# Kernel optimization log

Hardware: AMD Instinct MI355X
Metric: run time of the kernel (lower is better)

## Reference

```python
import math
import jax, jax.numpy as jnp
import numpy as np

B, H, Nt, Nl, E = 4, 16, 512, 512, 64
P = H * E  # 1024, pre-projection embedding dim


def setup_inputs() -> dict:
    key = jax.random.key(0)
    ks = jax.random.split(key, 8)
    return {
        "projected_u": jax.random.normal(ks[0], (B, H, Nt, P), jnp.float32),
        "projected_b": jax.random.normal(ks[1], (B, H, Nt, 1), jnp.float32),
        "mu": jax.random.normal(ks[2], (B, Nl, P), jnp.float32),
        "logvar": jax.random.normal(ks[3], (B, Nl, P), jnp.float32) * 0.5,
        "pi": jax.random.uniform(ks[4], (B, Nl, 1), jnp.float32, 1e-3, 1.0),
        "w_v": jax.random.normal(ks[5], (H, E, P), jnp.float32) * 0.02,
        "b_v": jax.random.normal(ks[6], (H, E, Nl), jnp.float32) * 0.02,
        "attn_mask": jnp.zeros((B * H, 1, Nl), dtype=bool),  # True = masked
    }


def reference(projected_u, projected_b, mu, logvar, pi, w_v, b_v, attn_mask):
    Bq, Hq, Ntq, Pq = projected_u.shape
    Nlq = mu.shape[1]
    Eq = w_v.shape[1]
    prior_var_u = math.sqrt(Eq)

    var = jnp.exp(logvar)                         # [B,Nl,P]
    biased_var = var + prior_var_u                # [B,Nl,P]

    # float additive mask [B*H,1,Nl]: -inf where attn_mask True or pi<=0
    pi_rep = jnp.repeat(pi, Hq, axis=0)           # [B*H,Nl,1]
    am = jnp.where(attn_mask, -jnp.inf, 0.0)
    am = am + jnp.where(pi_rep.transpose(0, 2, 1) <= 0, -jnp.inf, 0.0)
    masked = jnp.isneginf(am).transpose(0, 2, 1)  # [B*H,Nl,1]

    # scores [B,H,Nt,Nl]
    attn = jnp.einsum('bhmp,bnp->bhmn', projected_u, mu / biased_var) + projected_b

    pi_c = jnp.maximum(pi_rep, jnp.finfo(pi_rep.dtype).tiny)
    t1 = jnp.where(masked, 0.0, jnp.log(pi_c))                                  # [B*H,Nl,1]
    t2 = 0.5 * jnp.sum((mu / jnp.sqrt(biased_var)) ** 2, axis=-1, keepdims=True)  # [B,Nl,1]
    t2 = jnp.repeat(t2, Hq, axis=0)                                             # [B*H,Nl,1]
    t3 = jnp.where(masked, 0.0, jnp.log(jnp.repeat(biased_var, Hq, axis=0)))    # [B*H,Nl,P]
    t3 = jnp.sum(0.5 * t3, axis=-1, keepdims=True)                              # [B*H,Nl,1]

    attn = attn + (t1 - t2 - t3).reshape(Bq, Hq, Nlq, 1).transpose(0, 1, 3, 2)  # [B,H,1,Nl]
    attn = attn + am.reshape(Bq, Hq, 1, Nlq)
    attn = jax.nn.softmax(attn, axis=-1)                                        # [B,H,Nt,Nl]

    # denoised values: interpolation between query projection and means
    out = (jnp.einsum('bhmn,bnp->bhmp', attn, var / biased_var) * projected_u
           + jnp.einsum('bhmn,bnp->bhmp', attn, (prior_var_u / biased_var) * mu))  # [B,H,Nt,P]
    out = (jnp.einsum('bhmp,hep->bhme', out, w_v)
           + jnp.einsum('bhmn,hen->bhme', attn, b_v))                              # [B,H,Nt,E]
    return (out.reshape(Bq * Hq, Ntq, Eq), attn.reshape(Bq * Hq, Ntq, Nlq))
```

## Files before the change

### kernel.cpp

```cpp
#include <hip/hip_runtime.h>
#include <cstdint>
#include <cstddef>
#include <cmath>

#define B_  4
#define H_  16
#define NT  512
#define NL  512
#define E_  64
#define P_  1024
#define HE  1024
#define BH  64

typedef __attribute__((ext_vector_type(8))) short short8;
typedef __attribute__((ext_vector_type(8))) unsigned short ushort8;
typedef __attribute__((ext_vector_type(4))) float f32x4;
typedef unsigned short u16;

#define MFMA(a, b, c) __builtin_amdgcn_mfma_f32_16x16x32_bf16(a, b, c, 0, 0, 0)

static __device__ inline u16 f2bf_rne(float f) {
  unsigned u = __float_as_uint(f);
  unsigned r = u + 0x7FFFu + ((u >> 16) & 1u);
  return (u16)(r >> 16);
}

static __device__ inline void gl_lds16(const void* g, void* l) {
  __builtin_amdgcn_global_load_lds(
      (const __attribute__((address_space(1))) void*)g,
      (__attribute__((address_space(3))) void*)l, 16, 0, 0);
}

__global__ __launch_bounds__(256) void k_precompute(
    const float* __restrict__ mu, const float* __restrict__ logvar,
    const float* __restrict__ pi, u16* __restrict__ mobv_hi,
    u16* __restrict__ mobv_lo, u16* __restrict__ ibv,
    float* __restrict__ bias) {
  const int bn = blockIdx.x;
  const int t = threadIdx.x;
  const size_t base = (size_t)bn * P_;
  float t2 = 0.f, t3 = 0.f;
#pragma unroll
  for (int i = 0; i < P_ / 256; ++i) {
    const int p = t + i * 256;
    const float lv  = logvar[base + p];
    const float v   = expf(lv);
    const float bv  = v + 8.0f;
    const float inv = 1.0f / bv;
    const float m   = mu[base + p];
    const float x   = m * inv;
    const unsigned bits = __float_as_uint(x);
    mobv_hi[base + p] = (u16)(bits >> 16);
    const float r = x - __uint_as_float(bits & 0xFFFF0000u);
    mobv_lo[base + p] = (u16)(__float_as_uint(r) >> 16);
    ibv[base + p] = f2bf_rne(inv);
    t2 += m * x;
    t3 += logf(bv);
  }
  __shared__ float r2[256];
  __shared__ float r3[256];
  r2[t] = t2; r3[t] = t3;
  __syncthreads();
  for (int s = 128; s > 0; s >>= 1) {
    if (t < s) { r2[t] += r2[t + s]; r3[t] += r3[t + s]; }
    __syncthreads();
  }
  if (t == 0) {
    const float pv = pi[bn];
    float bb;
    if (pv <= 0.f) bb = -INFINITY;
    else bb = logf(fmaxf(pv, 1.17549435e-38f)) - 0.5f * r2[0] - 0.5f * r3[0];
    bias[bn] = bb;
  }
}

__global__ __launch_bounds__(256) void k_tr(const u16* __restrict__ ibv,
                                            u16* __restrict__ ibvT) {
  const int b  = blockIdx.z;
  const int p0 = blockIdx.x * 64;
  const int n0 = blockIdx.y * 64;
  const int t  = threadIdx.x;
  __shared__ u16 T[64][65];
  {
    const int ln = t >> 2, lp = (t & 3) * 16;
    const u16* src = ibv + ((size_t)b * NL + n0 + ln) * P_ + p0 + lp;
    const ushort8 v0 = *(const ushort8*)(src);
    const ushort8 v1 = *(const ushort8*)(src + 8);
#pragma unroll
    for (int j = 0; j < 8; ++j) { T[ln][lp + j] = v0[j]; T[ln][lp + 8 + j] = v1[j]; }
  }
  __syncthreads();
  {
    const int lp = t >> 2, ln = (t & 3) * 16;
    u16* dst = ibvT + ((size_t)b * P_ + p0 + lp) * NL + n0 + ln;
    ushort8 o0, o1;
#pragma unroll
    for (int j = 0; j < 8; ++j) { o0[j] = T[ln + j][lp]; o1[j] = T[ln + 8 + j][lp]; }
    *(ushort8*)(dst)     = o0;
    *(ushort8*)(dst + 8) = o1;
  }
}

__global__ __launch_bounds__(256) void k_wvcast(const float* __restrict__ wv,
                                                u16* __restrict__ wvb) {
  const int i = (blockIdx.x * 256 + threadIdx.x) * 4;
  const float4 f = *(const float4*)&wv[i];
  wvb[i + 0] = f2bf_rne(f.x);
  wvb[i + 1] = f2bf_rne(f.y);
  wvb[i + 2] = f2bf_rne(f.z);
  wvb[i + 3] = f2bf_rne(f.w);
}

__global__ __launch_bounds__(256) void k_w2p(
    const u16* __restrict__ mobv_hi, const u16* __restrict__ mobv_lo,
    const u16* __restrict__ wvb, const float* __restrict__ bv_,
    u16* __restrict__ W2pT) {
  const int b    = blockIdx.z;
  const int row0 = blockIdx.x * 64;
  const int col0 = blockIdx.y * 128;
  const int t = threadIdx.x;
  const int wave = t >> 6, lane = t & 63;
  const int l16 = lane & 15, sel = lane >> 4;
  const int mrow = (wave >> 1) * 32, ncol = (wave & 1) * 64;

  __shared__ u16 Ah[64 * 32];
  __shared__ u16 Al[64 * 32];
  __shared__ u16 Bs[128 * 32];

  const u16* Abh = mobv_hi + ((size_t)b * NL + row0) * P_;
  const u16* Abl = mobv_lo + ((size_t)b * NL + row0) * P_;
  const u16* Bb  = wvb + (size_t)col0 * P_;

  f32x4 acc[2][4];
#pragma unroll
  for (int i = 0; i < 2; ++i)
#pragma unroll
    for (int j = 0; j < 4; ++j) acc[i][j] = (f32x4){0.f, 0.f, 0.f, 0.f};

  for (int k0 = 0; k0 < P_; k0 += 32) {
    {
      const int c = t;
      const int row = c >> 2, k8 = (c & 3) ^ ((row >> 1) & 3);
      gl_lds16(Abh + (size_t)row * P_ + k0 + k8 * 8, &Ah[wave * 64 * 8]);
      gl_lds16(Abl + (size_t)row * P_ + k0 + k8 * 8, &Al[wave * 64 * 8]);
    }
#pragma unroll
    for (int i = 0; i < 2; ++i) {
      const int c = t + i * 256;
      const int row = c >> 2, k8 = (c & 3) ^ ((row >> 1) & 3);
      gl_lds16(Bb + (size_t)row * P_ + k0 + k8 * 8,
               &Bs[(i * 256 + wave * 64) * 8]);
    }
    __syncthreads();
    short8 ah[2], al[2], bf[4];
#pragma unroll
    for (int mt = 0; mt < 2; ++mt) {
      const int r = mrow + mt * 16 + l16;
      const int ch = sel ^ ((r >> 1) & 3);
      ah[mt] = *(const short8*)&Ah[r * 32 + ch * 8];
      al[mt] = *(const short8*)&Al[r * 32 + ch * 8];
    }
#pragma unroll
    for (int nt = 0; nt < 4; ++nt) {
      const int r = ncol + nt * 16 + l16;
      const int ch = sel ^ ((r >> 1) & 3);
      bf[nt] = *(const short8*)&Bs[r * 32 + ch * 8];
    }
#pragma unroll
    for (int mt = 0; mt < 2; ++mt)
#pragma unroll
      for (int nt = 0; nt < 4; ++nt) {
        acc[mt][nt] = MFMA(ah[mt], bf[nt], acc[mt][nt]);
        acc[mt][nt] = MFMA(al[mt], bf[nt], acc[mt][nt]);
      }
    __syncthreads();
  }
#pragma unroll
  for (int mt = 0; mt < 2; ++mt) {
    const int nbase = row0 + mrow + mt * 16 + sel * 4;
#pragma unroll
    for (int nt = 0; nt < 4; ++nt) {
      const int he = col0 + ncol + nt * 16 + l16;
      const float4 bvv = *(const float4*)&bv_[(size_t)he * NL + nbase];
      ushort4 o;
      o.x = f2bf_rne(8.0f * acc[mt][nt][0] + bvv.x);
      o.y = f2bf_rne(8.0f * acc[mt][nt][1] + bvv.y);
      o.z = f2bf_rne(8.0f * acc[mt][nt][2] + bvv.z);
      o.w = f2bf_rne(8.0f * acc[mt][nt][3] + bvv.w);
      *(ushort4*)&W2pT[((size_t)b * HE + he) * NL + nbase] = o;
    }
  }
}

__global__ __launch_bounds__(256) void k_scores(
    const float* __restrict__ U, const u16* __restrict__ mobv_hi,
    const u16* __restrict__ mobv_lo, const float* __restrict__ pb,
    const float* __restrict__ bias, const uint8_t* __restrict__ mask,
    float* __restrict__ attn) {
  const int b    = blockIdx.z;
  const int row0 = blockIdx.x * 128;
  const int col0 = blockIdx.y * 128;
  const int t = threadIdx.x;
  const int wave = t >> 6, lane = t & 63;
  const int l16 = lane & 15, sel = lane >> 4;
  const int mrow = wave * 32;

  __shared__ float Af[2][128 * 32];
  __shared__ u16   Bh[2][128 * 32];
  __shared__ u16   Bl[2][128 * 32];

  const float* Ab  = U + ((size_t)b * 8192 + row0) * P_;
  const u16*   Bbh = mobv_hi + ((size_t)b * NL + col0) * P_;
  const u16*   Bbl = mobv_lo + ((size_t)b * NL + col0) * P_;

  f32x4 acc[2][8];
#pragma unroll
  for (int i = 0; i < 2; ++i)
#pragma unroll
    for (int j = 0; j < 8; ++j) acc[i][j] = (f32x4){0.f, 0.f, 0.f, 0.f};

  auto stage = [&](int buf, int k0) {
#pragma unroll
    for (int i = 0; i < 4; ++i) {
      const int c = t + i * 256;
      const int row = c >> 3, k4 = (c & 7) ^ (row & 7);
      gl_lds16(Ab + (size_t)row * P_ + k0 + k4 * 4,
               &Af[buf][(i * 256 + wave * 64) * 4]);
    }
#pragma unroll
    for (int i = 0; i < 2; ++i) {
      const int c = t + i * 256;
      const int row = c >> 2, k8 = (c & 3) ^ ((row >> 1) & 3);
      gl_lds16(Bbh + (size_t)row * P_ + k0 + k8 * 8,
               &Bh[buf][(i * 256 + wave * 64) * 8]);
      gl_lds16(Bbl + (size_t)row * P_ + k0 + k8 * 8,
               &Bl[buf][(i * 256 + wave * 64) * 8]);
    }
  };

  stage(0, 0);
  __syncthreads();
  int cur = 0;
  for (int k0 = 0; k0 < P_; k0 += 32) {
    if (k0 + 32 < P_) stage(cur ^ 1, k0 + 32);

    short8 ah[2], al[2], bh[8], bl[8];
#pragma unroll
    for (int mt = 0; mt < 2; ++mt) {
      const int r = mrow + mt * 16 + l16;
      const int c0 = (sel * 2) ^ (r & 7);
      const int c1 = (sel * 2 + 1) ^ (r & 7);
      const float4 f0 = *(const float4*)&Af[cur][r * 32 + c0 * 4];
      const float4 f1 = *(const float4*)&Af[cur][r * 32 + c1 * 4];
      const float fv[8] = {f0.x, f0.y, f0.z, f0.w, f1.x, f1.y, f1.z, f1.w};
#pragma unroll
      for (int j = 0; j < 8; ++j) {
        const unsigned bits = __float_as_uint(fv[j]);
        ah[mt][j] = (short)(bits >> 16);
        const float rr = fv[j] - __uint_as_float(bits & 0xFFFF0000u);
        al[mt][j] = (short)(__float_as_uint(rr) >> 16);
      }
    }
#pragma unroll
    for (int nt = 0; nt < 8; ++nt) {
      const int r = nt * 16 + l16;
      const int ch = sel ^ ((r >> 1) & 3);
      bh[nt] = *(const short8*)&Bh[cur][r * 32 + ch * 8];
      bl[nt] = *(const short8*)&Bl[cur][r * 32 + ch * 8];
    }
#pragma unroll
    for (int mt = 0; mt < 2; ++mt)
#pragma unroll
      for (int nt = 0; nt < 8; ++nt) {
        acc[mt][nt] = MFMA(ah[mt], bh[nt], acc[mt][nt]);
        acc[mt][nt] = MFMA(ah[mt], bl[nt], acc[mt][nt]);
        acc[mt][nt] = MFMA(al[mt], bh[nt], acc[mt][nt]);
      }
    __syncthreads();
    cur ^= 1;
  }

  const int bh_ = b * H_ + (row0 >> 9);
  float pbv[2][4];
#pragma unroll
  for (int mt = 0; mt < 2; ++mt)
#pragma unroll
    for (int r = 0; r < 4; ++r)
      pbv[mt][r] = pb[(size_t)b * 8192 + row0 + mrow + mt * 16 + sel * 4 + r];
#pragma unroll
  for (int nt = 0; nt < 8; ++nt) {
    const int n = col0 + nt * 16 + l16;
    const float bcol = bias[b * NL + n];
    const bool mk = mask[(size_t)bh_ * NL + n] != 0;
#pragma unroll
    for (int mt = 0; mt < 2; ++mt) {
#pragma unroll
      for (int r = 0; r < 4; ++r) {
        const int row = row0 + mrow + mt * 16 + sel * 4 + r;
        float s = acc[mt][nt][r] + pbv[mt][r] + bcol;
        if (mk) s = -INFINITY;
        attn[((size_t)b * 8192 + row) * NL + n] = s;
      }
    }
  }
}

__global__ __launch_bounds__(256) void k_softmax(float* __restrict__ attn,
                                                 u16* __restrict__ attn_bf) {
  const int t = threadIdx.x;
  const int wave = t >> 6, lane = t & 63;
  const size_t r = (size_t)blockIdx.x * 4 + wave;
  float* row = attn + r * NL;
  const float4 v0 = ((const float4*)row)[lane * 2];
  const float4 v1 = ((const float4*)row)[lane * 2 + 1];
  float m = fmaxf(fmaxf(fmaxf(v0.x, v0.y), fmaxf(v0.z, v0.w)),
                  fmaxf(fmaxf(v1.x, v1.y), fmaxf(v1.z, v1.w)));
#pragma unroll
  for (int off = 32; off > 0; off >>= 1) m = fmaxf(m, __shfl_xor(m, off, 64));
  float e[8];
  e[0] = expf(v0.x - m); e[1] = expf(v0.y - m);
  e[2] = expf(v0.z - m); e[3] = expf(v0.w - m);
  e[4] = expf(v1.x - m); e[5] = expf(v1.y - m);
  e[6] = expf(v1.z - m); e[7] = expf(v1.w - m);
  float s = ((e[0] + e[1]) + (e[2] + e[3])) + ((e[4] + e[5]) + (e[6] + e[7]));
#pragma unroll
  for (int off = 32; off > 0; off >>= 1) s += __shfl_xor(s, off, 64);
  const float inv = 1.0f / s;
  float4 o0, o1;
  o0.x = e[0] * inv; o0.y = e[1] * inv; o0.z = e[2] * inv; o0.w = e[3] * inv;
  o1.x = e[4] * inv; o1.y = e[5] * inv; o1.z = e[6] * inv; o1.w = e[7] * inv;
  ((float4*)row)[lane * 2] = o0;
  ((float4*)row)[lane * 2 + 1] = o1;
  ushort4 b0, b1;
  b0.x = f2bf_rne(o0.x); b0.y = f2bf_rne(o0.y);
  b0.z = f2bf_rne(o0.z); b0.w = f2bf_rne(o0.w);
  b1.x = f2bf_rne(o1.x); b1.y = f2bf_rne(o1.y);
  b1.z = f2bf_rne(o1.z); b1.w = f2bf_rne(o1.w);
  ((ushort4*)(attn_bf + r * NL))[lane * 2] = b0;
  ((ushort4*)(attn_bf + r * NL))[lane * 2 + 1] = b1;
}

__global__ __launch_bounds__(256) void k_mid(
    const u16* __restrict__ attn_bf, const u16* __restrict__ ibvT,
    const float* __restrict__ U, u16* __restrict__ opS) {
  const int b    = blockIdx.z;
  const int row0 = blockIdx.x * 128;
  const int col0 = blockIdx.y * 128;
  const int t = threadIdx.x;
  const int wave = t >> 6, lane = t & 63;
  const int l16 = lane & 15, sel = lane >> 4;
  const int mrow = (wave >> 1) * 64, ncol = (wave & 1) * 64;

  __shared__ u16 As[128 * 32];
  __shared__ u16 Bs[128 * 32];

  const u16* Ab = attn_bf + ((size_t)b * 8192 + row0) * NL;
  const u16* Bb = ibvT + ((size_t)b * P_ + col0) * NL;

  f32x4 acc[4][4];
#pragma unroll
  for (int i = 0; i < 4; ++i)
#pragma unroll
    for (int j = 0; j < 4; ++j) acc[i][j] = (f32x4){0.f, 0.f, 0.f, 0.f};

  for (int k0 = 0; k0 < NL; k0 += 32) {
#pragma unroll
    for (int i = 0; i < 2; ++i) {
      const int c = t + i * 256;
      const int row = c >> 2, k8 = (c & 3) ^ ((row >> 1) & 3);
      gl_lds16(Ab + (size_t)row * NL + k0 + k8 * 8,
               &As[(i * 256 + wave * 64) * 8]);
      gl_lds16(Bb + (size_t)row * NL + k0 + k8 * 8,
               &Bs[(i * 256 + wave * 64) * 8]);
    }
    __syncthreads();
    short8 af[4], bf[4];
#pragma unroll
    for (int mt = 0; mt < 4; ++mt) {
      const int r = mrow + mt * 16 + l16;
      const int ch = sel ^ ((r >> 1) & 3);
      af[mt] = *(const short8*)&As[r * 32 + ch * 8];
    }
#pragma unroll
    for (int nt = 0; nt < 4; ++nt) {
      const int r = ncol + nt * 16 + l16;
      const int ch = sel ^ ((r >> 1) & 3);
      bf[nt] = *(const short8*)&Bs[r * 32 + ch * 8];
    }
#pragma unroll
    for (int mt = 0; mt < 4; ++mt)
#pragma unroll
      for (int nt = 0; nt < 4; ++nt)
        acc[mt][nt] = MFMA(af[mt], bf[nt], acc[mt][nt]);
    __syncthreads();
  }

#pragma unroll
  for (int mt = 0; mt < 4; ++mt) {
#pragma unroll
    for (int r = 0; r < 4; ++r) {
      const int m = row0 + mrow + mt * 16 + sel * 4 + r;
      const float* Urow = U + ((size_t)b * 8192 + m) * P_;
      u16* orow = opS + ((size_t)b * 8192 + m) * P_;
#pragma unroll
      for (int nt = 0; nt < 4; ++nt) {
        const int p = col0 + ncol + nt * 16 + l16;
        const float u = Urow[p];
        orow[p] = f2bf_rne((1.0f - 8.0f * acc[mt][nt][r]) * u);
      }
    }
  }
}

__global__ __launch_bounds__(256) void k_out2(
    const u16* __restrict__ opS, const u16* __restrict__ attn_bf,
    const u16* __restrict__ wvb, const u16* __restrict__ W2pT,
    float* __restrict__ out) {
  const int bh = blockIdx.y;
  const int b = bh >> 4, h = bh & 15;
  const int row0g = bh * NT + blockIdx.x * 64;
  const int t = threadIdx.x;
  const int wave = t >> 6, lane = t & 63;
  const int l16 = lane & 15, sel = lane >> 4;
  const int mrow = (wave >> 1) * 32, ncol = (wave & 1) * 32;

  __shared__ u16 As[64 * 64];
  __shared__ u16 Bs[64 * 64];

  f32x4 acc[2][2];
#pragma unroll
  for (int i = 0; i < 2; ++i)
#pragma unroll
    for (int j = 0; j < 2; ++j) acc[i][j] = (f32x4){0.f, 0.f, 0.f, 0.f};

  const u16* Ab1 = opS + (size_t)row0g * P_;
  const u16* Bb1 = wvb + (size_t)(h * 64) * P_;
  for (int k0 = 0; k0 < P_; k0 += 64) {
#pragma unroll
    for (int i = 0; i < 2; ++i) {
      const int c = t + i * 256;
      const int row = c >> 3, k8 = (c & 7) ^ (row & 7);
      gl_lds16(Ab1 + (size_t)row * P_ + k0 + k8 * 8,
               &As[(i * 256 + wave * 64) * 8]);
      gl_lds16(Bb1 + (size_t)row * P_ + k0 + k8 * 8,
               &Bs[(i * 256 + wave * 64) * 8]);
    }
    __syncthreads();
    short8 af[2][2], bf[2][2];
#pragma unroll
    for (int mt = 0; mt < 2; ++mt) {
      const int r = mrow + mt * 16 + l16;
#pragma unroll
      for (int kk = 0; kk < 2; ++kk) {
        const int ch = (kk * 4 + sel) ^ (r & 7);
        af[mt][kk] = *(const short8*)&As[r * 64 + ch * 8];
      }
    }
#pragma unroll
    for (int nt = 0; nt < 2; ++nt) {
      const int r = ncol + nt * 16 + l16;
#pragma unroll
      for (int kk = 0; kk < 2; ++kk) {
        const int ch = (kk * 4 + sel) ^ (r & 7);
        bf[nt][kk] = *(const short8*)&Bs[r * 64 + ch * 8];
      }
    }
#pragma unroll
    for (int mt = 0; mt < 2; ++mt)
#pragma unroll
      for (int nt = 0; nt < 2; ++nt) {
        acc[mt][nt] = MFMA(af[mt][0], bf[nt][0], acc[mt][nt]);
        acc[mt][nt] = MFMA(af[mt][1], bf[nt][1], acc[mt][nt]);
      }
    __syncthreads();
  }

  const u16* Ab2 = attn_bf + (size_t)row0g * NL;
  const u16* Bb2 = W2pT + ((size_t)b * HE + h * 64) * NL;
  for (int k0 = 0; k0 < NL; k0 += 64) {
#pragma unroll
    for (int i = 0; i < 2; ++i) {
      const int c = t + i * 256;
      const int row = c >> 3, k8 = (c & 7) ^ (row & 7);
      gl_lds16(Ab2 + (size_t)row * NL + k0 + k8 * 8,
               &As[(i * 256 + wave * 64) * 8]);
      gl_lds16(Bb2 + (size_t)row * NL + k0 + k8 * 8,
               &Bs[(i * 256 + wave * 64) * 8]);
    }
    __syncthreads();
    short8 af[2][2], bf[2][2];
#pragma unroll
    for (int mt = 0; mt < 2; ++mt) {
      const int r = mrow + mt * 16 + l16;
#pragma unroll
      for (int kk = 0; kk < 2; ++kk) {
        const int ch = (kk * 4 + sel) ^ (r & 7);
        af[mt][kk] = *(const short8*)&As[r * 64 + ch * 8];
      }
    }
#pragma unroll
    for (int nt = 0; nt < 2; ++nt) {
      const int r = ncol + nt * 16 + l16;
#pragma unroll
      for (int kk = 0; kk < 2; ++kk) {
        const int ch = (kk * 4 + sel) ^ (r & 7);
        bf[nt][kk] = *(const short8*)&Bs[r * 64 + ch * 8];
      }
    }
#pragma unroll
    for (int mt = 0; mt < 2; ++mt)
#pragma unroll
      for (int nt = 0; nt < 2; ++nt) {
        acc[mt][nt] = MFMA(af[mt][0], bf[nt][0], acc[mt][nt]);
        acc[mt][nt] = MFMA(af[mt][1], bf[nt][1], acc[mt][nt]);
      }
    __syncthreads();
  }

#pragma unroll
  for (int mt = 0; mt < 2; ++mt)
#pragma unroll
    for (int nt = 0; nt < 2; ++nt)
#pragma unroll
      for (int r = 0; r < 4; ++r) {
        const int row = row0g + mrow + mt * 16 + sel * 4 + r;
        const int e = ncol + nt * 16 + l16;
        out[(size_t)row * E_ + e] = acc[mt][nt][r];
      }
}

extern "C" void kernel_launch(void* const* d_in, const int* in_sizes, int n_in,
                              void* d_out, int out_size, void* d_ws, size_t ws_size,
                              hipStream_t stream) {
  const float*   u    = (const float*)d_in[0];
  const float*   pb   = (const float*)d_in[1];
  const float*   mu   = (const float*)d_in[2];
  const float*   logv = (const float*)d_in[3];
  const float*   pi   = (const float*)d_in[4];
  const float*   wv   = (const float*)d_in[5];
  const float*   bv   = (const float*)d_in[6];
  const uint8_t* mask = (const uint8_t*)d_in[7];

  float* out  = (float*)d_out;
  float* attn = out + (size_t)BH * NT * E_;

  u16*   mobv_hi = (u16*)d_ws;
  u16*   mobv_lo = mobv_hi + (size_t)B_ * NL * P_;
  u16*   ibvT    = mobv_lo + (size_t)B_ * NL * P_;
  u16*   W2pT    = ibvT + (size_t)B_ * P_ * NL;
  u16*   wvb     = W2pT + (size_t)B_ * HE * NL;
  float* bias    = (float*)(wvb + (size_t)HE * P_);
  u16*   attn_bf = (u16*)(bias + (size_t)B_ * NL);
  u16*   opS     = attn_bf + (size_t)BH * NT * NL;
  u16*   ibv     = opS;

  k_precompute<<<B_ * NL, 256, 0, stream>>>(mu, logv, pi, mobv_hi, mobv_lo,
                                            ibv, bias);
  k_tr<<<dim3(P_ / 64, NL / 64, B_), 256, 0, stream>>>(ibv, ibvT);
  k_wvcast<<<(HE * P_) / 1024, 256, 0, stream>>>(wv, wvb);
  k_w2p<<<dim3(NL / 64, HE / 128, B_), 256, 0, stream>>>(mobv_hi, mobv_lo, wvb,
                                                         bv, W2pT);
  k_scores<<<dim3(8192 / 128, NL / 128, B_), 256, 0, stream>>>(
      u, mobv_hi, mobv_lo, pb, bias, mask, attn);
  k_softmax<<<(B_ * H_ * NT) / 4, 256, 0, stream>>>(attn, attn_bf);
  k_mid<<<dim3(8192 / 128, P_ / 128, B_), 256, 0, stream>>>(attn_bf, ibvT, u,
                                                            opS);
  k_out2<<<dim3(NT / 64, BH), 256, 0, stream>>>(opS, attn_bf, wvb, W2pT, out);
}
```

Baseline: 464.9 us.

## Fuse mid and output GEMMs into one kernel, keeping intermediate in LDS

Merges k_mid (attn·ibvT times U) and k_out2 (projection by w_v plus attn·W2pT) into a single kernel. Each block now produces the 64×1024 intermediate in 128-column chunks, writes each chunk to LDS as bf16 and multiplies it straight into the E=64 output accumulator. This removes the global write and reread of the large opS buffer. The trade-off is a smaller 64-row M tile per block, so attn_bf is re-read once for each of the 8 P-chunks, and LDS use grows, which may lower occupancy. Separately, k_precompute is vectorised to float4 loads and ushort4 stores.

```diff
diff --git a/kernel.cpp b/kernel.cpp
--- a/kernel.cpp
+++ b/kernel.cpp
@@ -39,24 +39,37 @@
   const int bn = blockIdx.x;
   const int t = threadIdx.x;
   const size_t base = (size_t)bn * P_;
+  const int p = t * 4;
+  const float4 lv4 = *(const float4*)&logvar[base + p];
+  const float4 m4  = *(const float4*)&mu[base + p];
   float t2 = 0.f, t3 = 0.f;
-#pragma unroll
-  for (int i = 0; i < P_ / 256; ++i) {
-    const int p = t + i * 256;
-    const float lv  = logvar[base + p];
-    const float v   = expf(lv);
-    const float bv  = v + 8.0f;
-    const float inv = 1.0f / bv;
-    const float m   = mu[base + p];
-    const float x   = m * inv;
-    const unsigned bits = __float_as_uint(x);
-    mobv_hi[base + p] = (u16)(bits >> 16);
-    const float r = x - __uint_as_float(bits & 0xFFFF0000u);
-    mobv_lo[base + p] = (u16)(__float_as_uint(r) >> 16);
-    ibv[base + p] = f2bf_rne(inv);
-    t2 += m * x;
-    t3 += logf(bv);
-  }
+  ushort4 ohi, olo, oib;
+  {
+    const float lvv[4] = {lv4.x, lv4.y, lv4.z, lv4.w};
+    const float mvv[4] = {m4.x, m4.y, m4.z, m4.w};
+    u16 hi[4], lo[4], ib[4];
+#pragma unroll
+    for (int j = 0; j < 4; ++j) {
+      const float v   = expf(lvv[j]);
+      const float bv  = v + 8.0f;
+      const float inv = 1.0f / bv;
+      const float m   = mvv[j];
+      const float x   = m * inv;
+      const unsigned bits = __float_as_uint(x);
+      hi[j] = (u16)(bits >> 16);
+      const float r = x - __uint_as_float(bits & 0xFFFF0000u);
+      lo[j] = (u16)(__float_as_uint(r) >> 16);
+      ib[j] = f2bf_rne(inv);
+      t2 += m * x;
+      t3 += logf(bv);
+    }
+    ohi = make_ushort4(hi[0], hi[1], hi[2], hi[3]);
+    olo = make_ushort4(lo[0], lo[1], lo[2], lo[3]);
+    oib = make_ushort4(ib[0], ib[1], ib[2], ib[3]);
+  }
+  *(ushort4*)&mobv_hi[base + p] = ohi;
+  *(ushort4*)&mobv_lo[base + p] = olo;
+  *(ushort4*)&ibv[base + p]     = oib;
   __shared__ float r2[256];
   __shared__ float r3[256];
   r2[t] = t2; r3[t] = t3;
@@ -340,193 +353,121 @@
   ((ushort4*)(attn_bf + r * NL))[lane * 2 + 1] = b1;
 }
 
-__global__ __launch_bounds__(256) void k_mid(
+__global__ __launch_bounds__(256) void k_fused(
     const u16* __restrict__ attn_bf, const u16* __restrict__ ibvT,
-    const float* __restrict__ U, u16* __restrict__ opS) {
-  const int b    = blockIdx.z;
-  const int row0 = blockIdx.x * 128;
-  const int col0 = blockIdx.y * 128;
+    const float* __restrict__ U, const u16* __restrict__ wvb,
+    const u16* __restrict__ W2pT, float* __restrict__ out) {
+  const int bh = blockIdx.y;
+  const int b = bh >> 4, h = bh & 15;
+  const int m0g = bh * NT + blockIdx.x * 64;
   const int t = threadIdx.x;
   const int wave = t >> 6, lane = t & 63;
   const int l16 = lane & 15, sel = lane >> 4;
-  const int mrow = (wave >> 1) * 64, ncol = (wave & 1) * 64;
-
-  __shared__ u16 As[128 * 32];
+  const int w16 = wave * 16;
+
+  __shared__ u16 As[64 * 32];
   __shared__ u16 Bs[128 * 32];
-
-  const u16* Ab = attn_bf + ((size_t)b * 8192 + row0) * NL;
-  const u16* Bb = ibvT + ((size_t)b * P_ + col0) * NL;
-
-  f32x4 acc[4][4];
-#pragma unroll
-  for (int i = 0; i < 4; ++i)
-#pragma unroll
-    for (int j = 0; j < 4; ++j) acc[i][j] = (f32x4){0.f, 0.f, 0.f, 0.f};
-
+  __shared__ u16 Wv[64 * 128];
+  __shared__ u16 Ts[64 * 136];
+
+  f32x4 oacc[4];
+#pragma unroll
+  for (int j = 0; j < 4; ++j) oacc[j] = (f32x4){0.f, 0.f, 0.f, 0.f};
+
+  const u16* Abase = attn_bf + (size_t)m0g * NL;
+  const u16* Bibv  = ibvT + (size_t)b * P_ * NL;
+  const u16* Wbase = wvb + (size_t)(h * 64) * P_;
+
+  const int arow_f = w16 + l16;
+  const int ach    = sel ^ ((arow_f >> 1) & 3);
+
+  for (int q = 0; q < 8; ++q) {
+    const int p0 = q * 128;
+#pragma unroll
+    for (int i = 0; i < 4; ++i) {
+      const int c = t + i * 256;
+      const int row = c >> 4, k8 = (c & 15) ^ (row & 15);
+      gl_lds16(Wbase + (size_t)row * P_ + p0 + k8 * 8,
+               &Wv[(i * 256 + wave * 64) * 8]);
+    }
+    f32x4 sacc[8];
+#pragma unroll
+    for (int j = 0; j < 8; ++j) sacc[j] = (f32x4){0.f, 0.f, 0.f, 0.f};
+    for (int k0 = 0; k0 < NL; k0 += 32) {
+      {
+        const int row = t >> 2, k8 = (t & 3) ^ ((row >> 1) & 3);
+        gl_lds16(Abase + (size_t)row * NL + k0 + k8 * 8, &As[wave * 64 * 8]);
+      }
+#pragma unroll
+      for (int i = 0; i < 2; ++i) {
+        const int c = t + i * 256;
+        const int row = c >> 2, k8 = (c & 3) ^ ((row >> 1) & 3);
+        gl_lds16(Bibv + (size_t)(p0 + row) * NL + k0 + k8 * 8,
+                 &Bs[(i * 256 + wave * 64) * 8]);
+      }
+      __syncthreads();
+      const short8 a = *(const short8*)&As[arow_f * 32 + ach * 8];
+      short8 bf[8];
+#pragma unroll
+      for (int nt = 0; nt < 8; ++nt) {
+        const int r = nt * 16 + l16;
+        const int ch = sel ^ ((r >> 1) & 3);
+        bf[nt] = *(const short8*)&Bs[r * 32 + ch * 8];
+      }
+#pragma unroll
+      for (int nt = 0; nt < 8; ++nt) sacc[nt] = MFMA(a, bf[nt], sacc[nt]);
+      __syncthreads();
+    }
+#pragma unroll
+    for (int nt = 0; nt < 8; ++nt) {
+#pragma unroll
+      for (int r = 0; r < 4; ++r) {
+        const int row_rel = w16 + sel * 4 + r;
+        const int prel = nt * 16 + l16;
+        const float u = U[(size_t)(m0g + row_rel) * P_ + p0 + prel];
+        Ts[row_rel * 136 + prel] = f2bf_rne((1.0f - 8.0f * sacc[nt][r]) * u);
+      }
+    }
+#pragma unroll
+    for (int kk = 0; kk < 4; ++kk) {
+      const short8 a = *(const short8*)&Ts[arow_f * 136 + (kk * 4 + sel) * 8];
+#pragma unroll
+      for (int ne = 0; ne < 4; ++ne) {
+        const int re = ne * 16 + l16;
+        const int ch = (kk * 4 + sel) ^ (re & 15);
+        const short8 bf = *(const short8*)&Wv[re * 128 + ch * 8];
+        oacc[ne] = MFMA(a, bf, oacc[ne]);
+      }
+    }
+    __syncthreads();
+  }
+
+  const u16* W2base = W2pT + ((size_t)b * HE + h * 64) * NL;
   for (int k0 = 0; k0 < NL; k0 += 32) {
-#pragma unroll
-    for (int i = 0; i < 2; ++i) {
-      const int c = t + i * 256;
-      const int row = c >> 2, k8 = (c & 3) ^ ((row >> 1) & 3);
-      gl_lds16(Ab + (size_t)row * NL + k0 + k8 * 8,
-               &As[(i * 256 + wave * 64) * 8]);
-      gl_lds16(Bb + (size_t)row * NL + k0 + k8 * 8,
-               &Bs[(i * 256 + wave * 64) * 8]);
-    }
-    __syncthreads();
-    short8 af[4], bf[4];
-#pragma unroll
-    for (int mt = 0; mt < 4; ++mt) {
-      const int r = mrow + mt * 16 + l16;
-      const int ch = sel ^ ((r >> 1) & 3);
-      af[mt] = *(const short8*)&As[r * 32 + ch * 8];
-    }
-#pragma unroll
-    for (int nt = 0; nt < 4; ++nt) {
-      const int r = ncol + nt * 16 + l16;
-      const int ch = sel ^ ((r >> 1) & 3);
-      bf[nt] = *(const short8*)&Bs[r * 32 + ch * 8];
-    }
-#pragma unroll
-    for (int mt = 0; mt < 4; ++mt)
-#pragma unroll
-      for (int nt = 0; nt < 4; ++nt)
-        acc[mt][nt] = MFMA(af[mt], bf[nt], acc[mt][nt]);
-    __syncthreads();
-  }
-
-#pragma unroll
-  for (int mt = 0; mt < 4; ++mt) {
+    {
+      const int row = t >> 2, k8 = (t & 3) ^ ((row >> 1) & 3);
+      gl_lds16(Abase + (size_t)row * NL + k0 + k8 * 8, &As[wave * 64 * 8]);
+      gl_lds16(W2base + (size_t)row * NL + k0 + k8 * 8, &Bs[wave * 64 * 8]);
+    }
+    __syncthreads();
+    const short8 a = *(const short8*)&As[arow_f * 32 + ach * 8];
+#pragma unroll
+    for (int ne = 0; ne < 4; ++ne) {
+      const int re = ne * 16 + l16;
+      const int ch = sel ^ ((re >> 1) & 3);
+      const short8 bf = *(const short8*)&Bs[re * 32 + ch * 8];
+      oacc[ne] = MFMA(a, bf, oacc[ne]);
+    }
+    __syncthreads();
+  }
+
+#pragma unroll
+  for (int ne = 0; ne < 4; ++ne)
 #pragma unroll
     for (int r = 0; r < 4; ++r) {
-      const int m = row0 + mrow + mt * 16 + sel * 4 + r;
-      const float* Urow = U + ((size_t)b * 8192 + m) * P_;
-      u16* orow = opS + ((size_t)b * 8192 + m) * P_;
-#pragma unroll
-      for (int nt = 0; nt < 4; ++nt) {
-        const int p = col0 + ncol + nt * 16 + l16;
-        const float u = Urow[p];
-        orow[p] = f2bf_rne((1.0f - 8.0f * acc[mt][nt][r]) * u);
-      }
-    }
-  }
-}
-
-__global__ __launch_bounds__(256) void k_out2(
-    const u16* __restrict__ opS, const u16* __restrict__ attn_bf,
-    const u16* __restrict__ wvb, const u16* __restrict__ W2pT,
-    float* __restrict__ out) {
-  const int bh = blockIdx.y;
-  const int b = bh >> 4, h = bh & 15;
-  const int row0g = bh * NT + blockIdx.x * 64;
-  const int t = threadIdx.x;
-  const int wave = t >> 6, lane = t & 63;
-  const int l16 = lane & 15, sel = lane >> 4;
-  const int mrow = (wave >> 1) * 32, ncol = (wave & 1) * 32;
-
-  __shared__ u16 As[64 * 64];
-  __shared__ u16 Bs[64 * 64];
-
-  f32x4 acc[2][2];
-#pragma unroll
-  for (int i = 0; i < 2; ++i)
-#pragma unroll
-    for (int j = 0; j < 2; ++j) acc[i][j] = (f32x4){0.f, 0.f, 0.f, 0.f};
-
-  const u16* Ab1 = opS + (size_t)row0g * P_;
-  const u16* Bb1 = wvb + (size_t)(h * 64) * P_;
-  for (int k0 = 0; k0 < P_; k0 += 64) {
-#pragma unroll
-    for (int i = 0; i < 2; ++i) {
-      const int c = t + i * 256;
-      const int row = c >> 3, k8 = (c & 7) ^ (row & 7);
-      gl_lds16(Ab1 + (size_t)row * P_ + k0 + k8 * 8,
-               &As[(i * 256 + wave * 64) * 8]);
-      gl_lds16(Bb1 + (size_t)row * P_ + k0 + k8 * 8,
-               &Bs[(i * 256 + wave * 64) * 8]);
-    }
-    __syncthreads();
-    short8 af[2][2], bf[2][2];
-#pragma unroll
-    for (int mt = 0; mt < 2; ++mt) {
-      const int r = mrow + mt * 16 + l16;
-#pragma unroll
-      for (int kk = 0; kk < 2; ++kk) {
-        const int ch = (kk * 4 + sel) ^ (r & 7);
-        af[mt][kk] = *(const short8*)&As[r * 64 + ch * 8];
-      }
-    }
-#pragma unroll
-    for (int nt = 0; nt < 2; ++nt) {
-      const int r = ncol + nt * 16 + l16;
-#pragma unroll
-      for (int kk = 0; kk < 2; ++kk) {
-        const int ch = (kk * 4 + sel) ^ (r & 7);
-        bf[nt][kk] = *(const short8*)&Bs[r * 64 + ch * 8];
-      }
-    }
-#pragma unroll
-    for (int mt = 0; mt < 2; ++mt)
-#pragma unroll
-      for (int nt = 0; nt < 2; ++nt) {
-        acc[mt][nt] = MFMA(af[mt][0], bf[nt][0], acc[mt][nt]);
-        acc[mt][nt] = MFMA(af[mt][1], bf[nt][1], acc[mt][nt]);
-      }
-    __syncthreads();
-  }
-
-  const u16* Ab2 = attn_bf + (size_t)row0g * NL;
-  const u16* Bb2 = W2pT + ((size_t)b * HE + h * 64) * NL;
-  for (int k0 = 0; k0 < NL; k0 += 64) {
-#pragma unroll
-    for (int i = 0; i < 2; ++i) {
-      const int c = t + i * 256;
-      const int row = c >> 3, k8 = (c & 7) ^ (row & 7);
-      gl_lds16(Ab2 + (size_t)row * NL + k0 + k8 * 8,
-               &As[(i * 256 + wave * 64) * 8]);
-      gl_lds16(Bb2 + (size_t)row * NL + k0 + k8 * 8,
-               &Bs[(i * 256 + wave * 64) * 8]);
-    }
-    __syncthreads();
-    short8 af[2][2], bf[2][2];
-#pragma unroll
-    for (int mt = 0; mt < 2; ++mt) {
-      const int r = mrow + mt * 16 + l16;
-#pragma unroll
-      for (int kk = 0; kk < 2; ++kk) {
-        const int ch = (kk * 4 + sel) ^ (r & 7);
-        af[mt][kk] = *(const short8*)&As[r * 64 + ch * 8];
-      }
-    }
-#pragma unroll
-    for (int nt = 0; nt < 2; ++nt) {
-      const int r = ncol + nt * 16 + l16;
-#pragma unroll
-      for (int kk = 0; kk < 2; ++kk) {
-        const int ch = (kk * 4 + sel) ^ (r & 7);
-        bf[nt][kk] = *(const short8*)&Bs[r * 64 + ch * 8];
-      }
-    }
-#pragma unroll
-    for (int mt = 0; mt < 2; ++mt)
-#pragma unroll
-      for (int nt = 0; nt < 2; ++nt) {
-        acc[mt][nt] = MFMA(af[mt][0], bf[nt][0], acc[mt][nt]);
-        acc[mt][nt] = MFMA(af[mt][1], bf[nt][1], acc[mt][nt]);
-      }
-    __syncthreads();
-  }
-
-#pragma unroll
-  for (int mt = 0; mt < 2; ++mt)
-#pragma unroll
-    for (int nt = 0; nt < 2; ++nt)
-#pragma unroll
-      for (int r = 0; r < 4; ++r) {
-        const int row = row0g + mrow + mt * 16 + sel * 4 + r;
-        const int e = ncol + nt * 16 + l16;
-        out[(size_t)row * E_ + e] = acc[mt][nt][r];
-      }
+      const int row = m0g + w16 + sel * 4 + r;
+      out[(size_t)row * E_ + ne * 16 + l16] = oacc[ne][r];
+    }
 }
 
 extern "C" void kernel_launch(void* const* d_in, const int* in_sizes, int n_in,
@@ -551,8 +492,7 @@
   u16*   wvb     = W2pT + (size_t)B_ * HE * NL;
   float* bias    = (float*)(wvb + (size_t)HE * P_);
   u16*   attn_bf = (u16*)(bias + (size_t)B_ * NL);
-  u16*   opS     = attn_bf + (size_t)BH * NT * NL;
-  u16*   ibv     = opS;
+  u16*   ibv     = attn_bf + (size_t)BH * NT * NL;
 
   k_precompute<<<B_ * NL, 256, 0, stream>>>(mu, logv, pi, mobv_hi, mobv_lo,
                                             ibv, bias);
@@ -563,7 +503,6 @@
   k_scores<<<dim3(8192 / 128, NL / 128, B_), 256, 0, stream>>>(
       u, mobv_hi, mobv_lo, pb, bias, mask, attn);
   k_softmax<<<(B_ * H_ * NT) / 4, 256, 0, stream>>>(attn, attn_bf);
-  k_mid<<<dim3(8192 / 128, P_ / 128, B_), 256, 0, stream>>>(attn_bf, ibvT, u,
-                                                            opS);
-  k_out2<<<dim3(NT / 64, BH), 256, 0, stream>>>(opS, attn_bf, wvb, W2pT, out);
-}
+  k_fused<<<dim3(NT / 64, BH), 256, 0, stream>>>(attn_bf, ibvT, u, wvb, W2pT,
+                                                 out);
+}
```

After: 476.9 us. 2.6% more time.
